# Kernel tuning notes

Measured on AMD Instinct MI355X. Metric: run time of the kernel, lower is better.

## Reference

```python
import jax, jax.numpy as jnp
import numpy as np

B, T, C = 4, 2048, 1024
N_HEAD = 16
HEAD_DIM = C // N_HEAD


def setup_inputs() -> dict:
    key = jax.random.key(0)
    k1, k2, k3 = jax.random.split(key, 3)
    x = jax.random.normal(k1, (B, T, C), dtype=jnp.float32)
    # torch Linear(n_embd, 3*n_embd, bias=False): weight [out,in]; store transposed [in,out]
    w_qkv = jax.random.normal(k2, (C, 3 * C), dtype=jnp.float32) * (1.0 / np.sqrt(C))
    w_proj = jax.random.normal(k3, (C, C), dtype=jnp.float32) * (1.0 / np.sqrt(C))
    return {"x": x, "w_qkv": w_qkv, "w_proj": w_proj}


def reference(x, w_qkv, w_proj):
    Bb, Tt, Cc = x.shape
    qkv = x @ w_qkv  # [B,T,3C]
    q, k, v = jnp.split(qkv, 3, axis=2)
    # [B,T,H,D] -> [B,H,T,D]
    def heads(t):
        return t.reshape(Bb, Tt, N_HEAD, HEAD_DIM).transpose(0, 2, 1, 3)
    q, k, v = heads(q), heads(k), heads(v)
    att = jnp.einsum("bhqd,bhkd->bhqk", q, k) / jnp.sqrt(jnp.float32(HEAD_DIM))
    causal = jnp.tril(jnp.ones((Tt, Tt), dtype=bool))
    att = jnp.where(causal, att, -jnp.inf)
    att = jax.nn.softmax(att, axis=-1)
    y = jnp.einsum("bhqk,bhkd->bhqd", att, v)  # [B,H,T,D]
    y = y.transpose(0, 2, 1, 3).reshape(Bb, Tt, Cc)
    return y @ w_proj
```

## Files before the change

### kernel.cpp

```cpp
#include <hip/hip_runtime.h>
#include <hip/hip_bf16.h>

typedef unsigned short u16;
typedef __bf16 bf16x8 __attribute__((ext_vector_type(8)));
typedef float f32x4 __attribute__((ext_vector_type(4)));
typedef float f32x16 __attribute__((ext_vector_type(16)));
typedef unsigned short u16x8 __attribute__((ext_vector_type(8)));
typedef unsigned short u16x4 __attribute__((ext_vector_type(4)));
typedef unsigned int u32x4 __attribute__((ext_vector_type(4)));

__device__ __forceinline__ u16 f2bf(float f) {
  unsigned u = __builtin_bit_cast(unsigned, f);
  u += 0x7FFFu + ((u >> 16) & 1u);
  return (u16)(u >> 16);
}

__device__ __forceinline__ unsigned cvt_pk_bf16(float lo, float hi_) {
  unsigned r;
  asm("v_cvt_pk_bf16_f32 %0, %1, %2" : "=v"(r) : "v"(lo), "v"(hi_));
  return r;
}

#define GLD16(gp, lp)                                                          \
  __builtin_amdgcn_global_load_lds(                                            \
      (const __attribute__((address_space(1))) void*)(gp),                     \
      (__attribute__((address_space(3))) void*)(lp), 16, 0, 0)


__global__ __launch_bounds__(256) void cast_f32_bf16(
    const float* __restrict__ in, u16* __restrict__ out, int n4) {
  int i = blockIdx.x * 256 + threadIdx.x;
  if (i >= n4) return;
  float4 v = ((const float4*)in)[i];
  u16x4 o = {f2bf(v.x), f2bf(v.y), f2bf(v.z), f2bf(v.w)};
  *(u16x4*)(out + (size_t)i * 4) = o;
}

__global__ __launch_bounds__(256) void transpose_cast(
    const float* __restrict__ in, u16* __restrict__ out, int R, int C) {
  __shared__ float t[32][33];
  int c0 = blockIdx.x * 32, r0 = blockIdx.y * 32;
  int tx = threadIdx.x, ty = threadIdx.y;
#pragma unroll
  for (int k = 0; k < 4; ++k)
    t[ty + 8 * k][tx] = in[(size_t)(r0 + ty + 8 * k) * C + c0 + tx];
  __syncthreads();
#pragma unroll
  for (int k = 0; k < 4; ++k)
    out[(size_t)(c0 + ty + 8 * k) * R + r0 + tx] = f2bf(t[tx][ty + 8 * k]);
}


template <int EPI>
__global__ __launch_bounds__(256) void gemm_bt(
    const u16* __restrict__ A, const u16* __restrict__ Bt, int K,
    u16* __restrict__ Qd, u16* __restrict__ Kd, u16* __restrict__ Vd,
    float* __restrict__ Od, int N) {
  __shared__ u16 As[128 * 32];
  __shared__ u16 Bs[128 * 32];
  int tid = threadIdx.x;
  int l = tid & 63, w = tid >> 6;
  int wr = w >> 1, wc = w & 1;
  int lr = l & 15, lg = l >> 4;
  int m0 = blockIdx.y * 128, n0 = blockIdx.x * 128;

  f32x4 acc[4][4];
  f32x4 z4 = {0.f, 0.f, 0.f, 0.f};
#pragma unroll
  for (int mi = 0; mi < 4; ++mi)
#pragma unroll
    for (int ni = 0; ni < 4; ++ni) acc[mi][ni] = z4;

  for (int kt = 0; kt < K; kt += 32) {
#pragma unroll
    for (int it = 0; it < 2; ++it) {
      int q = it * 256 + tid;
      int r = q >> 2, s = q & 3;
      int sw = (s ^ (r & 3)) << 3;
      GLD16(A + (size_t)(m0 + r) * K + kt + sw, As + it * 2048 + w * 512);
      GLD16(Bt + (size_t)(n0 + r) * K + kt + sw, Bs + it * 2048 + w * 512);
    }
    __syncthreads();

    bf16x8 af[4], bfv[4];
#pragma unroll
    for (int mi = 0; mi < 4; ++mi) {
      int row = wr * 64 + mi * 16 + lr;
      af[mi] = *(const bf16x8*)&As[row * 32 + ((lg ^ (row & 3)) << 3)];
    }
#pragma unroll
    for (int ni = 0; ni < 4; ++ni) {
      int col = wc * 64 + ni * 16 + lr;
      bfv[ni] = *(const bf16x8*)&Bs[col * 32 + ((lg ^ (col & 3)) << 3)];
    }
#pragma unroll
    for (int mi = 0; mi < 4; ++mi)
#pragma unroll
      for (int ni = 0; ni < 4; ++ni)
        acc[mi][ni] = __builtin_amdgcn_mfma_f32_16x16x32_bf16(
            af[mi], bfv[ni], acc[mi][ni], 0, 0, 0);
    __syncthreads();
  }

  if (EPI == 0) {
    int s_blk = n0 >> 10;
    u16* dst = (s_blk == 0) ? Qd : ((s_blk == 1) ? Kd : Vd);
#pragma unroll
    for (int mi = 0; mi < 4; ++mi)
#pragma unroll
      for (int ni = 0; ni < 4; ++ni)
#pragma unroll
        for (int i = 0; i < 4; ++i) {
          int m = m0 + wr * 64 + mi * 16 + lg * 4 + i;
          int n = n0 + wc * 64 + ni * 16 + lr;
          int b = m >> 11, t = m & 2047;
          int c = n & 1023, h = c >> 6, d = c & 63;
          dst[((size_t)(b * 16 + h) * 2048 + t) * 64 + d] = f2bf(acc[mi][ni][i]);
        }
  } else {
#pragma unroll
    for (int mi = 0; mi < 4; ++mi)
#pragma unroll
      for (int ni = 0; ni < 4; ++ni)
#pragma unroll
        for (int i = 0; i < 4; ++i) {
          int m = m0 + wr * 64 + mi * 16 + lg * 4 + i;
          int n = n0 + wc * 64 + ni * 16 + lr;
          Od[(size_t)m * N + n] = acc[mi][ni][i];
        }
  }
}


__global__ __launch_bounds__(512, 2) void attn_fwd(
    const u16* __restrict__ Qg, const u16* __restrict__ Kg,
    const u16* __restrict__ Vg, u16* __restrict__ Yg) {
  __shared__ u16 Ks[2][64 * 64];
  __shared__ u16 Vt[64 * 64];

  int tid = threadIdx.x;
  int l = tid & 63, w = tid >> 6;
  int l31 = l & 31, hi = l >> 5, l7 = l & 7;
  int bid = blockIdx.x;
  int pp = bid >> 6;
  int bh = bid & 63;
  const u16* Qb = Qg + (size_t)bh * 131072;
  const u16* Kb = Kg + (size_t)bh * 131072;
  const u16* Vb = Vg + (size_t)bh * 131072;
  int b = bh >> 4, h = bh & 15;

  int vt_ = tid >> 3, vdq = tid & 7;
  int kr = tid >> 3, ks8 = tid & 7;

#pragma unroll 1
  for (int ph = 0; ph < 2; ++ph) {
    int qt = ph ? (7 - pp) : pp;
    int q0w = qt * 256 + w * 32;
    int jn = 4 * qt + 3;

    bf16x8 qreg[4];
#pragma unroll
    for (int ds = 0; ds < 4; ++ds)
      qreg[ds] =
          *(const bf16x8*)(Qb + (size_t)(q0w + l31) * 64 + ds * 16 + hi * 8);

    f32x16 o_acc[2];
#pragma unroll
    for (int dt = 0; dt < 2; ++dt)
#pragma unroll
      for (int r = 0; r < 16; ++r) o_acc[dt][r] = 0.f;
    float m_run = -3e38f, l_run = 0.f;

    u16x8 va;
    GLD16(Kb + (size_t)kr * 64 + ((ks8 ^ (kr & 7)) << 3), &Ks[0][0] + w * 512);
    va = *(const u16x8*)(Vb + (size_t)vt_ * 64 + vdq * 8);

    for (int j = 0; j <= jn; ++j) {
      int kv0 = j * 64;
      const u16* ksb = Ks[j & 1];
#pragma unroll
      for (int jj = 0; jj < 8; ++jj) {
        int d = vdq * 8 + jj;
        Vt[d * 64 + (((vt_ >> 3) ^ jj ^ vdq) << 3) + (vt_ & 7)] = va[jj];
      }
      __syncthreads();

      if (j < jn) {
        int kv1 = kv0 + 64;
        GLD16(Kb + (size_t)(kv1 + kr) * 64 + ((ks8 ^ (kr & 7)) << 3),
              &Ks[(j + 1) & 1][0] + w * 512);
        va = *(const u16x8*)(Vb + (size_t)(kv1 + vt_) * 64 + vdq * 8);
      }

      bool active = kv0 <= q0w + 31;
      if (active) {
        int qg = q0w + l31;
        bf16x8 kf[2][4];
#pragma unroll
        for (int kt = 0; kt < 2; ++kt)
#pragma unroll
          for (int ds = 0; ds < 4; ++ds)
            kf[kt][ds] = *(const bf16x8*)&ksb[(32 * kt + l31) * 64 +
                                              (((2 * ds + hi) ^ l7) << 3)];
        f32x16 sa[2];
        __builtin_amdgcn_s_setprio(1);
#pragma unroll
        for (int kt = 0; kt < 2; ++kt) {
          f32x16 acc;
#pragma unroll
          for (int r = 0; r < 16; ++r) acc[r] = 0.f;
#pragma unroll
          for (int ds = 0; ds < 4; ++ds)
            acc = __builtin_amdgcn_mfma_f32_32x32x16_bf16(kf[kt][ds], qreg[ds],
                                                          acc, 0, 0, 0);
          sa[kt] = acc;
        }
        __builtin_amdgcn_s_setprio(0);

        float mloc = -3e38f;
        if (kv0 + 63 > q0w) {
#pragma unroll
          for (int kt = 0; kt < 2; ++kt)
#pragma unroll
            for (int r = 0; r < 16; ++r) {
              int kg = kv0 + kt * 32 + ((r & 3) + 8 * (r >> 2) + 4 * hi);
              float v = sa[kt][r];
              v = (kg <= qg) ? v : -8e30f;
              sa[kt][r] = v;
              mloc = fmaxf(mloc, v);
            }
        } else {
#pragma unroll
          for (int kt = 0; kt < 2; ++kt)
#pragma unroll
            for (int r = 0; r < 16; ++r) mloc = fmaxf(mloc, sa[kt][r]);
        }
        float mx = fmaxf(mloc, __shfl_xor(mloc, 32)) * 0.125f;
        if (!__all(mx <= m_run + 8.f)) {
          float mn = fmaxf(m_run, mx);
          float fsc = __expf(m_run - mn);
          m_run = mn;
          l_run *= fsc;
#pragma unroll
          for (int r = 0; r < 16; ++r) {
            float fv = __shfl(fsc, (r & 3) + 8 * (r >> 2) + 4 * hi + 32 * hi);
            o_acc[0][r] *= fv;
            o_acc[1][r] *= fv;
          }
        }
        float mm = m_run * 1.44269504f;
        float lloc = 0.f;
#pragma unroll
        for (int kt = 0; kt < 2; ++kt)
#pragma unroll
          for (int r = 0; r < 16; ++r) {
            float p = exp2f(__builtin_fmaf(sa[kt][r], 0.18033688f, -mm));
            sa[kt][r] = p;
            lloc += p;
          }
        l_run += lloc + __shfl_xor(lloc, 32);
        unsigned pk0[8], pk1[8];
#pragma unroll
        for (int m = 0; m < 8; ++m) {
          pk0[m] = cvt_pk_bf16(sa[0][2 * m], sa[0][2 * m + 1]);
          pk1[m] = cvt_pk_bf16(sa[1][2 * m], sa[1][2 * m + 1]);
        }
        bf16x8 vf[2][4];
#pragma unroll
        for (int dt = 0; dt < 2; ++dt)
#pragma unroll
          for (int ks = 0; ks < 4; ++ks) {
            int d = 32 * dt + l31;
            int ch = ((2 * ks + hi) ^ (d & 7) ^ ((d >> 3) & 7)) & 7;
            vf[dt][ks] = *(const bf16x8*)&Vt[d * 64 + (ch << 3)];
          }
#pragma unroll
        for (int ks = 0; ks < 4; ++ks) {
          int c0 = 4 * (ks & 1);
          unsigned a0 = (ks < 2) ? pk0[c0] : pk1[c0];
          unsigned a1 = (ks < 2) ? pk0[c0 + 1] : pk1[c0 + 1];
          unsigned a2 = (ks < 2) ? pk0[c0 + 2] : pk1[c0 + 2];
          unsigned a3 = (ks < 2) ? pk0[c0 + 3] : pk1[c0 + 3];
          unsigned pubX = hi ? a0 : a2;
          unsigned pubY = hi ? a1 : a3;
          unsigned rx = (unsigned)__shfl_xor((int)pubX, 32);
          unsigned ry = (unsigned)__shfl_xor((int)pubY, 32);
          u32x4 fa;
          fa.x = hi ? rx : a0;
          fa.y = hi ? ry : a1;
          fa.z = hi ? a2 : rx;
          fa.w = hi ? a3 : ry;
          bf16x8 paf = __builtin_bit_cast(bf16x8, fa);
          __builtin_amdgcn_s_setprio(1);
#pragma unroll
          for (int dt = 0; dt < 2; ++dt)
            o_acc[dt] = __builtin_amdgcn_mfma_f32_32x32x16_bf16(
                paf, vf[dt][ks], o_acc[dt], 0, 0, 0);
          __builtin_amdgcn_s_setprio(0);
        }
      }
      __syncthreads();
    }

#pragma unroll
    for (int r = 0; r < 16; ++r) {
      int crow = (r & 3) + 8 * (r >> 2) + 4 * hi;
      float li = __shfl(l_run, crow + 32 * hi);
      float inv = 1.f / li;
      int q = q0w + crow;
#pragma unroll
      for (int dt = 0; dt < 2; ++dt) {
        float y = o_acc[dt][r] * inv;
        Yg[(size_t)(b * 2048 + q) * 1024 + h * 64 + dt * 32 + l31] = f2bf(y);
      }
    }
  }
}


extern "C" void kernel_launch(void* const* d_in, const int* in_sizes, int n_in,
                              void* d_out, int out_size, void* d_ws, size_t ws_size,
                              hipStream_t stream) {
  const float* x = (const float*)d_in[0];
  const float* w_qkv = (const float*)d_in[1];
  const float* w_proj = (const float*)d_in[2];
  float* out = (float*)d_out;
  u16* ws = (u16*)d_ws;

  u16* xb = ws;
  u16* wq = xb + 8388608;
  u16* wp = wq + 3145728;
  u16* Qb = wp + 1048576;
  u16* Kb = Qb + 8388608;
  u16* Vb = Kb + 8388608;
  u16* Yb = xb;

  cast_f32_bf16<<<8192, 256, 0, stream>>>(x, xb, 2097152);
  transpose_cast<<<dim3(96, 32), dim3(32, 8), 0, stream>>>(w_qkv, wq, 1024, 3072);
  transpose_cast<<<dim3(32, 32), dim3(32, 8), 0, stream>>>(w_proj, wp, 1024, 1024);
  gemm_bt<0><<<dim3(24, 64), 256, 0, stream>>>(xb, wq, 1024, Qb, Kb, Vb, nullptr, 3072);
  attn_fwd<<<256, 512, 0, stream>>>(Qb, Kb, Vb, Yb);
  gemm_bt<1><<<dim3(8, 64), 256, 0, stream>>>(Yb, wp, 1024, nullptr, nullptr, nullptr, out, 1024);
}
```

Measured before the change: 205.1 us.

## Software-pipeline attention PV with next QK tile; deepen GEMM K-tile to 64

The attention loop is restructured into a two-stage software pipeline. The P·V MFMAs of the previous KV tile now run alongside the QK^T MFMAs and softmax of the current tile, using double-buffered V-transpose LDS and a packed P register buffer, plus an epilogue that drains the last tile. Separately, the projection GEMMs load 64-wide K slices with an 8-way XOR swizzle, which halves the barrier count per K. The aim is to overlap matrix work with softmax VALU work and cut sync overhead, at the cost of more LDS and register pressure.

```diff
diff --git a/kernel.cpp b/kernel.cpp
--- a/kernel.cpp
+++ b/kernel.cpp
@@ -56,8 +56,8 @@
     const u16* __restrict__ A, const u16* __restrict__ Bt, int K,
     u16* __restrict__ Qd, u16* __restrict__ Kd, u16* __restrict__ Vd,
     float* __restrict__ Od, int N) {
-  __shared__ u16 As[128 * 32];
-  __shared__ u16 Bs[128 * 32];
+  __shared__ u16 As[128 * 64];
+  __shared__ u16 Bs[128 * 64];
   int tid = threadIdx.x;
   int l = tid & 63, w = tid >> 6;
   int wr = w >> 1, wc = w & 1;
@@ -71,34 +71,37 @@
 #pragma unroll
     for (int ni = 0; ni < 4; ++ni) acc[mi][ni] = z4;
 
-  for (int kt = 0; kt < K; kt += 32) {
-#pragma unroll
-    for (int it = 0; it < 2; ++it) {
+  for (int kt = 0; kt < K; kt += 64) {
+#pragma unroll
+    for (int it = 0; it < 4; ++it) {
       int q = it * 256 + tid;
-      int r = q >> 2, s = q & 3;
-      int sw = (s ^ (r & 3)) << 3;
+      int r = q >> 3, s = q & 7;
+      int sw = (s ^ (r & 7)) << 3;
       GLD16(A + (size_t)(m0 + r) * K + kt + sw, As + it * 2048 + w * 512);
       GLD16(Bt + (size_t)(n0 + r) * K + kt + sw, Bs + it * 2048 + w * 512);
     }
     __syncthreads();
 
-    bf16x8 af[4], bfv[4];
-#pragma unroll
-    for (int mi = 0; mi < 4; ++mi) {
-      int row = wr * 64 + mi * 16 + lr;
-      af[mi] = *(const bf16x8*)&As[row * 32 + ((lg ^ (row & 3)) << 3)];
-    }
-#pragma unroll
-    for (int ni = 0; ni < 4; ++ni) {
-      int col = wc * 64 + ni * 16 + lr;
-      bfv[ni] = *(const bf16x8*)&Bs[col * 32 + ((lg ^ (col & 3)) << 3)];
-    }
-#pragma unroll
-    for (int mi = 0; mi < 4; ++mi)
-#pragma unroll
-      for (int ni = 0; ni < 4; ++ni)
-        acc[mi][ni] = __builtin_amdgcn_mfma_f32_16x16x32_bf16(
-            af[mi], bfv[ni], acc[mi][ni], 0, 0, 0);
+#pragma unroll
+    for (int ks2 = 0; ks2 < 2; ++ks2) {
+      bf16x8 af[4], bfv[4];
+#pragma unroll
+      for (int mi = 0; mi < 4; ++mi) {
+        int row = wr * 64 + mi * 16 + lr;
+        af[mi] = *(const bf16x8*)&As[row * 64 + (((ks2 * 4 + lg) ^ (row & 7)) << 3)];
+      }
+#pragma unroll
+      for (int ni = 0; ni < 4; ++ni) {
+        int col = wc * 64 + ni * 16 + lr;
+        bfv[ni] = *(const bf16x8*)&Bs[col * 64 + (((ks2 * 4 + lg) ^ (col & 7)) << 3)];
+      }
+#pragma unroll
+      for (int mi = 0; mi < 4; ++mi)
+#pragma unroll
+        for (int ni = 0; ni < 4; ++ni)
+          acc[mi][ni] = __builtin_amdgcn_mfma_f32_16x16x32_bf16(
+              af[mi], bfv[ni], acc[mi][ni], 0, 0, 0);
+    }
     __syncthreads();
   }
 
@@ -132,11 +135,121 @@
 }
 
 
+#define ATTN_TILE(J, P)                                                        \
+  {                                                                            \
+    const int kv0 = (J) * 64;                                                  \
+    _Pragma("unroll") for (int jj = 0; jj < 8; ++jj) {        \
+      int d = vdq * 8 + jj;                                                    \
+      Vt[P][d * 64 + (((vt_ >> 3) ^ jj ^ vdq) << 3) + (vt_ & 7)] = va[jj];     \
+    }                                                                          \
+    __syncthreads();                       \
+    if ((J) < jn) {                                    \
+      GLD16(Kb + (size_t)(kv0 + 64 + kr) * 64 + ((ks8 ^ (kr & 7)) << 3),       \
+            &Ks[1 - (P)][0] + w * 512);                                        \
+      va = *(const u16x8*)(Vb + (size_t)(kv0 + 64 + vt_) * 64 + vdq * 8);      \
+    }                                                                          \
+    const bool act = kv0 <= q0w + 31;                                          \
+    const bool act_prev = (J) > 0 && (kv0 - 64) <= q0w + 31;                   \
+    f32x16 sa[2];                                                              \
+    if (act) {         \
+      bf16x8 kf[2][4];                                                         \
+      _Pragma("unroll") for (int kt = 0; kt < 2; ++kt)                         \
+          _Pragma("unroll") for (int ds = 0; ds < 4; ++ds)                     \
+              kf[kt][ds] = *(const bf16x8*)&Ks[P][(32 * kt + l31) * 64 +       \
+                                                  (((2 * ds + hi) ^ l7) << 3)];\
+      __builtin_amdgcn_s_setprio(1);                                           \
+      _Pragma("unroll") for (int kt = 0; kt < 2; ++kt) {                       \
+        f32x16 acc;                                                            \
+        _Pragma("unroll") for (int r = 0; r < 16; ++r) acc[r] = 0.f;           \
+        _Pragma("unroll") for (int ds = 0; ds < 4; ++ds)                       \
+            acc = __builtin_amdgcn_mfma_f32_32x32x16_bf16(kf[kt][ds],          \
+                                                          qreg[ds], acc,      \
+                                                          0, 0, 0);            \
+        sa[kt] = acc;                                                          \
+      }                                                                        \
+      __builtin_amdgcn_s_setprio(0);                                           \
+    }                                                                          \
+    if (act_prev) {                             \
+      bf16x8 vf[2][4];                                                         \
+      _Pragma("unroll") for (int dt = 0; dt < 2; ++dt)                         \
+          _Pragma("unroll") for (int ks = 0; ks < 4; ++ks) {                   \
+        int d = 32 * dt + l31;                                                 \
+        int ch = ((2 * ks + hi) ^ (d & 7) ^ ((d >> 3) & 7)) & 7;               \
+        vf[dt][ks] = *(const bf16x8*)&Vt[1 - (P)][d * 64 + (ch << 3)];         \
+      }                                                                        \
+      _Pragma("unroll") for (int ks = 0; ks < 4; ++ks) {                       \
+        const int base = (ks < 2) ? 0 : 8;                                     \
+        const int c0 = base + 4 * (ks & 1);                                    \
+        unsigned a0 = pk[1 - (P)][c0], a1 = pk[1 - (P)][c0 + 1];               \
+        unsigned a2 = pk[1 - (P)][c0 + 2], a3 = pk[1 - (P)][c0 + 3];           \
+        unsigned pubX = hi ? a0 : a2;                                          \
+        unsigned pubY = hi ? a1 : a3;                                          \
+        unsigned rx = (unsigned)__shfl_xor((int)pubX, 32);                     \
+        unsigned ry = (unsigned)__shfl_xor((int)pubY, 32);                     \
+        u32x4 fa;                                                              \
+        fa.x = hi ? rx : a0;                                                   \
+        fa.y = hi ? ry : a1;                                                   \
+        fa.z = hi ? a2 : rx;                                                   \
+        fa.w = hi ? a3 : ry;                                                   \
+        bf16x8 paf = __builtin_bit_cast(bf16x8, fa);                           \
+        __builtin_amdgcn_s_setprio(1);                                         \
+        _Pragma("unroll") for (int dt = 0; dt < 2; ++dt)                       \
+            o_acc[dt] = __builtin_amdgcn_mfma_f32_32x32x16_bf16(               \
+                paf, vf[dt][ks], o_acc[dt], 0, 0, 0);                          \
+        __builtin_amdgcn_s_setprio(0);                                         \
+      }                                                                        \
+    }                                                                          \
+    if (act) {         \
+      const int qg = q0w + l31;                                                \
+      float mloc = -3e38f;                                                     \
+      if (kv0 + 63 > q0w) {                                                    \
+        _Pragma("unroll") for (int kt = 0; kt < 2; ++kt)                       \
+            _Pragma("unroll") for (int r = 0; r < 16; ++r) {                   \
+          int kg = kv0 + kt * 32 + ((r & 3) + 8 * (r >> 2) + 4 * hi);          \
+          float v = sa[kt][r];                                                 \
+          v = (kg <= qg) ? v : -8e30f;                                         \
+          sa[kt][r] = v;                                                       \
+          mloc = fmaxf(mloc, v);                                               \
+        }                                                                      \
+      } else {                                                                 \
+        _Pragma("unroll") for (int kt = 0; kt < 2; ++kt)                       \
+            _Pragma("unroll") for (int r = 0; r < 16; ++r)                     \
+                mloc = fmaxf(mloc, sa[kt][r]);                                 \
+      }                                                                        \
+      float mx = fmaxf(mloc, __shfl_xor(mloc, 32)) * 0.125f;                   \
+      if (!__all(mx <= m_run + 8.f)) {                          \
+        float mn = fmaxf(m_run, mx);                                           \
+        float fsc = __expf(m_run - mn);                                        \
+        m_run = mn;                                                            \
+        l_run *= fsc;                                                          \
+        _Pragma("unroll") for (int r = 0; r < 16; ++r) {                       \
+          float fv = __shfl(fsc, (r & 3) + 8 * (r >> 2) + 4 * hi + 32 * hi);   \
+          o_acc[0][r] *= fv;                                                   \
+          o_acc[1][r] *= fv;                                                   \
+        }                                                                      \
+      }                                                                        \
+      float mm = m_run * 1.44269504f;                                          \
+      float lloc = 0.f;                                                        \
+      _Pragma("unroll") for (int kt = 0; kt < 2; ++kt)                         \
+          _Pragma("unroll") for (int r = 0; r < 16; ++r) {                     \
+        float p = exp2f(__builtin_fmaf(sa[kt][r], 0.18033688f, -mm));          \
+        sa[kt][r] = p;                                                         \
+        lloc += p;                                                             \
+      }                                                                        \
+      l_run += lloc + __shfl_xor(lloc, 32);                                    \
+      _Pragma("unroll") for (int m = 0; m < 8; ++m) {                          \
+        pk[P][m] = cvt_pk_bf16(sa[0][2 * m], sa[0][2 * m + 1]);                \
+        pk[P][8 + m] = cvt_pk_bf16(sa[1][2 * m], sa[1][2 * m + 1]);            \
+      }                                                                        \
+    }                                                                          \
+    __syncthreads();              \
+  }
+
 __global__ __launch_bounds__(512, 2) void attn_fwd(
     const u16* __restrict__ Qg, const u16* __restrict__ Kg,
     const u16* __restrict__ Vg, u16* __restrict__ Yg) {
   __shared__ u16 Ks[2][64 * 64];
-  __shared__ u16 Vt[64 * 64];
+  __shared__ u16 Vt[2][64 * 64];
 
   int tid = threadIdx.x;
   int l = tid & 63, w = tid >> 6;
@@ -170,136 +283,49 @@
 #pragma unroll
       for (int r = 0; r < 16; ++r) o_acc[dt][r] = 0.f;
     float m_run = -3e38f, l_run = 0.f;
+    unsigned pk[2][16];
 
     u16x8 va;
     GLD16(Kb + (size_t)kr * 64 + ((ks8 ^ (kr & 7)) << 3), &Ks[0][0] + w * 512);
     va = *(const u16x8*)(Vb + (size_t)vt_ * 64 + vdq * 8);
 
-    for (int j = 0; j <= jn; ++j) {
-      int kv0 = j * 64;
-      const u16* ksb = Ks[j & 1];
-#pragma unroll
-      for (int jj = 0; jj < 8; ++jj) {
-        int d = vdq * 8 + jj;
-        Vt[d * 64 + (((vt_ >> 3) ^ jj ^ vdq) << 3) + (vt_ & 7)] = va[jj];
+#pragma unroll 1
+    for (int j0 = 0; j0 <= jn; j0 += 2) {
+      ATTN_TILE(j0, 0)
+      ATTN_TILE(j0 + 1, 1)
+    }
+
+    if (jn * 64 <= q0w + 31) {
+      bf16x8 vf[2][4];
+#pragma unroll
+      for (int dt = 0; dt < 2; ++dt)
+#pragma unroll
+        for (int ks = 0; ks < 4; ++ks) {
+          int d = 32 * dt + l31;
+          int ch = ((2 * ks + hi) ^ (d & 7) ^ ((d >> 3) & 7)) & 7;
+          vf[dt][ks] = *(const bf16x8*)&Vt[1][d * 64 + (ch << 3)];
+        }
+#pragma unroll
+      for (int ks = 0; ks < 4; ++ks) {
+        const int base = (ks < 2) ? 0 : 8;
+        const int c0 = base + 4 * (ks & 1);
+        unsigned a0 = pk[1][c0], a1 = pk[1][c0 + 1];
+        unsigned a2 = pk[1][c0 + 2], a3 = pk[1][c0 + 3];
+        unsigned pubX = hi ? a0 : a2;
+        unsigned pubY = hi ? a1 : a3;
+        unsigned rx = (unsigned)__shfl_xor((int)pubX, 32);
+        unsigned ry = (unsigned)__shfl_xor((int)pubY, 32);
+        u32x4 fa;
+        fa.x = hi ? rx : a0;
+        fa.y = hi ? ry : a1;
+        fa.z = hi ? a2 : rx;
+        fa.w = hi ? a3 : ry;
+        bf16x8 paf = __builtin_bit_cast(bf16x8, fa);
+#pragma unroll
+        for (int dt = 0; dt < 2; ++dt)
+          o_acc[dt] = __builtin_amdgcn_mfma_f32_32x32x16_bf16(
+              paf, vf[dt][ks], o_acc[dt], 0, 0, 0);
       }
-      __syncthreads();
-
-      if (j < jn) {
-        int kv1 = kv0 + 64;
-        GLD16(Kb + (size_t)(kv1 + kr) * 64 + ((ks8 ^ (kr & 7)) << 3),
-              &Ks[(j + 1) & 1][0] + w * 512);
-        va = *(const u16x8*)(Vb + (size_t)(kv1 + vt_) * 64 + vdq * 8);
-      }
-
-      bool active = kv0 <= q0w + 31;
-      if (active) {
-        int qg = q0w + l31;
-        bf16x8 kf[2][4];
-#pragma unroll
-        for (int kt = 0; kt < 2; ++kt)
-#pragma unroll
-          for (int ds = 0; ds < 4; ++ds)
-            kf[kt][ds] = *(const bf16x8*)&ksb[(32 * kt + l31) * 64 +
-                                              (((2 * ds + hi) ^ l7) << 3)];
-        f32x16 sa[2];
-        __builtin_amdgcn_s_setprio(1);
-#pragma unroll
-        for (int kt = 0; kt < 2; ++kt) {
-          f32x16 acc;
-#pragma unroll
-          for (int r = 0; r < 16; ++r) acc[r] = 0.f;
-#pragma unroll
-          for (int ds = 0; ds < 4; ++ds)
-            acc = __builtin_amdgcn_mfma_f32_32x32x16_bf16(kf[kt][ds], qreg[ds],
-                                                          acc, 0, 0, 0);
-          sa[kt] = acc;
-        }
-        __builtin_amdgcn_s_setprio(0);
-
-        float mloc = -3e38f;
-        if (kv0 + 63 > q0w) {
-#pragma unroll
-          for (int kt = 0; kt < 2; ++kt)
-#pragma unroll
-            for (int r = 0; r < 16; ++r) {
-              int kg = kv0 + kt * 32 + ((r & 3) + 8 * (r >> 2) + 4 * hi);
-              float v = sa[kt][r];
-              v = (kg <= qg) ? v : -8e30f;
-              sa[kt][r] = v;
-              mloc = fmaxf(mloc, v);
-            }
-        } else {
-#pragma unroll
-          for (int kt = 0; kt < 2; ++kt)
-#pragma unroll
-            for (int r = 0; r < 16; ++r) mloc = fmaxf(mloc, sa[kt][r]);
-        }
-        float mx = fmaxf(mloc, __shfl_xor(mloc, 32)) * 0.125f;
-        if (!__all(mx <= m_run + 8.f)) {
-          float mn = fmaxf(m_run, mx);
-          float fsc = __expf(m_run - mn);
-          m_run = mn;
-          l_run *= fsc;
-#pragma unroll
-          for (int r = 0; r < 16; ++r) {
-            float fv = __shfl(fsc, (r & 3) + 8 * (r >> 2) + 4 * hi + 32 * hi);
-            o_acc[0][r] *= fv;
-            o_acc[1][r] *= fv;
-          }
-        }
-        float mm = m_run * 1.44269504f;
-        float lloc = 0.f;
-#pragma unroll
-        for (int kt = 0; kt < 2; ++kt)
-#pragma unroll
-          for (int r = 0; r < 16; ++r) {
-            float p = exp2f(__builtin_fmaf(sa[kt][r], 0.18033688f, -mm));
-            sa[kt][r] = p;
-            lloc += p;
-          }
-        l_run += lloc + __shfl_xor(lloc, 32);
-        unsigned pk0[8], pk1[8];
-#pragma unroll
-        for (int m = 0; m < 8; ++m) {
-          pk0[m] = cvt_pk_bf16(sa[0][2 * m], sa[0][2 * m + 1]);
-          pk1[m] = cvt_pk_bf16(sa[1][2 * m], sa[1][2 * m + 1]);
-        }
-        bf16x8 vf[2][4];
-#pragma unroll
-        for (int dt = 0; dt < 2; ++dt)
-#pragma unroll
-          for (int ks = 0; ks < 4; ++ks) {
-            int d = 32 * dt + l31;
-            int ch = ((2 * ks + hi) ^ (d & 7) ^ ((d >> 3) & 7)) & 7;
-            vf[dt][ks] = *(const bf16x8*)&Vt[d * 64 + (ch << 3)];
-          }
-#pragma unroll
-        for (int ks = 0; ks < 4; ++ks) {
-          int c0 = 4 * (ks & 1);
-          unsigned a0 = (ks < 2) ? pk0[c0] : pk1[c0];
-          unsigned a1 = (ks < 2) ? pk0[c0 + 1] : pk1[c0 + 1];
-          unsigned a2 = (ks < 2) ? pk0[c0 + 2] : pk1[c0 + 2];
-          unsigned a3 = (ks < 2) ? pk0[c0 + 3] : pk1[c0 + 3];
-          unsigned pubX = hi ? a0 : a2;
-          unsigned pubY = hi ? a1 : a3;
-          unsigned rx = (unsigned)__shfl_xor((int)pubX, 32);
-          unsigned ry = (unsigned)__shfl_xor((int)pubY, 32);
-          u32x4 fa;
-          fa.x = hi ? rx : a0;
-          fa.y = hi ? ry : a1;
-          fa.z = hi ? a2 : rx;
-          fa.w = hi ? a3 : ry;
-          bf16x8 paf = __builtin_bit_cast(bf16x8, fa);
-          __builtin_amdgcn_s_setprio(1);
-#pragma unroll
-          for (int dt = 0; dt < 2; ++dt)
-            o_acc[dt] = __builtin_amdgcn_mfma_f32_32x32x16_bf16(
-                paf, vf[dt][ks], o_acc[dt], 0, 0, 0);
-          __builtin_amdgcn_s_setprio(0);
-        }
-      }
-      __syncthreads();
     }
 
 #pragma unroll
```

Measured after the change: 212.3 us. 3.5% more time.
